# Performance work log

Hardware: AMD Instinct MI355X
Metric: run time of the kernel (lower is better)

Reference implementation:

```python
import jax, jax.numpy as jnp
import numpy as np

B, EMB, HT, WD = 32, 256, 56, 56
NH, WS, SHIFTED = 8, 4, True


def setup_inputs() -> dict:
    key = jax.random.key(0)
    ks = jax.random.split(key, 6)
    x = jax.random.normal(ks[0], (B, EMB, HT, WD), jnp.float32)
    s = 1.0 / np.sqrt(EMB)
    w1 = jax.random.uniform(ks[1], (3 * EMB, EMB), jnp.float32, -s, s)
    b1 = jax.random.uniform(ks[2], (3 * EMB,), jnp.float32, -s, s)
    w2 = jax.random.uniform(ks[3], (EMB, EMB), jnp.float32, -s, s)
    b2 = jax.random.uniform(ks[4], (EMB,), jnp.float32, -s, s)
    pos_emb = jax.random.normal(ks[5], (2 * WS - 1, 2 * WS - 1), jnp.float32)
    return {"x": x, "w1": w1, "b1": b1, "w2": w2, "b2": b2, "pos_emb": pos_emb}


def _rel_indices(ws):
    coords = np.array([[i, j] for i in range(ws) for j in range(ws)])
    rel = coords[None, :, :] - coords[:, None, :] + ws - 1  # (ws^2, ws^2, 2)
    return jnp.asarray(rel)


def _shift_masks(ws):
    m = np.zeros((ws * ws, ws * ws), np.float32)
    s = ws * (ws // 2)
    m[-s:, :-s] = -np.inf
    m[:-s, -s:] = -np.inf
    # '(r w1) (c w2) -> (w1 r) (w2 c)' with r=c=ws
    col = m.reshape(ws, ws, ws, ws).transpose(1, 0, 3, 2).reshape(ws * ws, ws * ws)
    return jnp.asarray(m), jnp.asarray(col)


def reference(x, w1, b1, w2, b2, pos_emb):
    b, c, ht, wd = x.shape
    ws, nh = WS, NH
    e = c // nh
    # b c h w -> b (h w) c, then QKV projection
    xt = x.reshape(b, c, ht * wd).transpose(0, 2, 1)
    qkv = xt @ w1.T + b1                      # (b, hw, 3c)
    # '(c k)' with c outer, k inner -> reshape (..., c, 3)
    qkv = qkv.reshape(b, ht, wd, c, 3)
    if SHIFTED:
        qkv = jnp.roll(qkv, (-ws // 2, -ws // 2), axis=(1, 2))
    Wh, Ww = ht // ws, wd // ws
    # 'b (Wh w1) (Ww w2) (e H) k -> b H Wh Ww (w1 w2) e k'  (e outer, H inner)
    qkv = qkv.reshape(b, Wh, ws, Ww, ws, e, nh, 3)
    qkv = qkv.transpose(0, 6, 1, 3, 2, 4, 5, 7).reshape(b, nh, Wh, Ww, ws * ws, e, 3)
    Q, K, V = qkv[..., 0], qkv[..., 1], qkv[..., 2]
    scale = jnp.sqrt(jnp.float32(c / nh))
    wei = jnp.einsum('bhijpe,bhijqe->bhijpq', Q, K) / scale  # (b,H,Wh,Ww,ws^2,ws^2)
    rel = _rel_indices(ws)
    wei = wei + pos_emb[rel[..., 0], rel[..., 1]]
    if SHIFTED:
        row_mask, col_mask = _shift_masks(ws)
        wei = wei.at[:, :, -1, :].add(row_mask)
        wei = wei.at[:, :, :, -1].add(col_mask)
    attn = jax.nn.softmax(wei, axis=-1)
    out = jnp.einsum('bhijpq,bhijqe->bhijpe', attn, V)
    # 'b H Wh Ww (w1 w2) e -> b (Wh w1) (Ww w2) (H e)'
    out = out.reshape(b, nh, Wh, Ww, ws, ws, e)
    out = out.transpose(0, 2, 4, 3, 5, 1, 6).reshape(b, ht, wd, nh * e)
    out = out.reshape(b, ht * wd, c)
    return out @ w2.T + b2
```

## Files before the change

### kernel.cpp

```cpp
#include <hip/hip_runtime.h>
#include <hip/hip_bf16.h>
#include <math.h>

typedef __attribute__((ext_vector_type(8))) short short8;
typedef __attribute__((ext_vector_type(4))) short short4_;
typedef __attribute__((ext_vector_type(4))) float f32x4;

#define B_    32
#define C_    256
#define HW_   3136
#define N1_   768
#define NWIN_ 14
#define M_    100352

__device__ __forceinline__ short bf16_of(float f) {
  union { __hip_bfloat16 h; short s; } u;
  u.h = __float2bfloat16(f);
  return u.s;
}

__device__ __forceinline__ void load_lds16(const void* g, void* l) {
  __builtin_amdgcn_global_load_lds(
      (const __attribute__((address_space(1))) unsigned int*)g,
      (__attribute__((address_space(3))) unsigned int*)l, 16, 0, 0);
}

__device__ __forceinline__ f32x4 mfma16x16x16bf16(short4_ a, short4_ b, f32x4 c) {
#if __has_builtin(__builtin_amdgcn_mfma_f32_16x16x16bf16_1k)
  return __builtin_amdgcn_mfma_f32_16x16x16bf16_1k(a, b, c, 0, 0, 0);
#else
  asm volatile("v_mfma_f32_16x16x16_bf16 %0, %1, %2, %0\n\ts_nop 7\n\ts_nop 7"
               : "+v"(c) : "v"(a), "v"(b));
  return c;
#endif
}

__global__ void conv_weights(const float* __restrict__ w1, const float* __restrict__ w2,
                             short* __restrict__ w1b, short* __restrict__ w2b) {
  int i = blockIdx.x * 256 + threadIdx.x;
  if (i < 196608) w1b[i] = bf16_of(w1[i]);
  if (i < 65536)  w2b[i] = bf16_of(w2[i]);
}

__global__ __launch_bounds__(256) void transpose_x(const float* __restrict__ x,
                                                   short* __restrict__ xt) {
  __shared__ short T[64 * 258];
  const int t = threadIdx.x;
  const int m0 = blockIdx.x * 64;
  const int b  = m0 / HW_;
  const int hw0 = m0 - b * HW_;

  for (int it = 0; it < 16; ++it) {
    const int c = it * 16 + (t >> 4);
    const int hw4 = (t & 15) * 4;
    float4 v = *(const float4*)(x + ((size_t)b * C_ + c) * HW_ + hw0 + hw4);
    T[(hw4 + 0) * 258 + c] = bf16_of(v.x);
    T[(hw4 + 1) * 258 + c] = bf16_of(v.y);
    T[(hw4 + 2) * 258 + c] = bf16_of(v.z);
    T[(hw4 + 3) * 258 + c] = bf16_of(v.w);
  }
  __syncthreads();
  for (int it = 0; it < 8; ++it) {
    const int idx = it * 256 + t;
    const int row = idx >> 5, ch = idx & 31;
    const short* rp = &T[row * 258 + ch * 8];
    int4 o;
    o.x = *(const int*)(rp + 0);
    o.y = *(const int*)(rp + 2);
    o.z = *(const int*)(rp + 4);
    o.w = *(const int*)(rp + 6);
    *(int4*)(xt + (size_t)(m0 + row) * C_ + ch * 8) = o;
  }
}

__global__ __launch_bounds__(256) void qkv_gemm(const short* __restrict__ xt,
    const short* __restrict__ w1b, const float* __restrict__ b1,
    short* __restrict__ qkvb) {
  __shared__ char smem[32768];
  char* As = smem;
  char* Bs = smem + 16384;
  const int t = threadIdx.x, l = t & 63, w = t >> 6;
  const int d = blockIdx.x, xcd = d & 7, i0 = d >> 3;
  const int bn = i0 % 6, bm = (i0 / 6) * 8 + xcd;
  const int m0 = bm * 128, n0 = bn * 128;
  const int lane = l & 15, kg = l >> 4;
  const int wm = w >> 1, wn = w & 1;

  f32x4 acc[4][4];
#pragma unroll
  for (int i = 0; i < 4; ++i)
#pragma unroll
    for (int j = 0; j < 4; ++j) acc[i][j] = (f32x4){0.f, 0.f, 0.f, 0.f};

  for (int ks = 0; ks < 4; ++ks) {
    const int k0 = ks * 64;
#pragma unroll
    for (int q = 0; q < 4; ++q) {
      const int row = (w * 4 + q) * 8 + (l >> 3);
      const int sc  = (l & 7) ^ (row & 7);
      load_lds16(xt  + (size_t)(m0 + row) * 256 + k0 + sc * 8, As + (w * 4 + q) * 1024);
      load_lds16(w1b + (size_t)(n0 + row) * 256 + k0 + sc * 8, Bs + (w * 4 + q) * 1024);
    }
    __syncthreads();
#pragma unroll
    for (int s = 0; s < 2; ++s) {
      short8 a[4], b[4];
#pragma unroll
      for (int i = 0; i < 4; ++i) {
        const int r = wm * 64 + i * 16 + lane;
        a[i] = *(const short8*)(As + r * 128 + ((s * 64 + kg * 16) ^ ((r & 7) << 4)));
      }
#pragma unroll
      for (int j = 0; j < 4; ++j) {
        const int r = wn * 64 + j * 16 + lane;
        b[j] = *(const short8*)(Bs + r * 128 + ((s * 64 + kg * 16) ^ ((r & 7) << 4)));
      }
#pragma unroll
      for (int i = 0; i < 4; ++i)
#pragma unroll
        for (int j = 0; j < 4; ++j)
          acc[i][j] = __builtin_amdgcn_mfma_f32_16x16x32_bf16(a[i], b[j], acc[i][j], 0, 0, 0);
    }
    __syncthreads();
  }

#pragma unroll
  for (int j = 0; j < 4; ++j) {
    const int n = n0 + wn * 64 + j * 16 + lane;
    const float bias = b1[n];
#pragma unroll
    for (int i = 0; i < 4; ++i) {
      const int mb = m0 + wm * 64 + i * 16 + kg * 4;
#pragma unroll
      for (int r = 0; r < 4; ++r)
        qkvb[(size_t)(mb + r) * N1_ + n] = bf16_of(acc[i][j][r] + bias);
    }
  }
}

__global__ __launch_bounds__(512) void win_attn(const short* __restrict__ qkvb,
    const float* __restrict__ pos, short* __restrict__ attnb) {
  __shared__ short Sq[16 * 776];
  __shared__ short Ot[16 * 272];
  __shared__ float Pe[49];

  const int t = threadIdx.x, l = t & 63, h = t >> 6;
  if (t < 49) Pe[t] = pos[t];

  const int win = blockIdx.x;
  const int wxi = win % NWIN_;
  const int wyi = (win / NWIN_) % NWIN_;
  const int b   = win / (NWIN_ * NWIN_);

#pragma unroll
  for (int rep = 0; rep < 3; ++rep) {
    const int idx = rep * 512 + t;
    const int row = idx / 96, ch = idx % 96;
    const int pr = row >> 2, pc = row & 3;
    int y  = wyi * 4 + pr + 2; if (y >= 56) y -= 56;
    int xx = wxi * 4 + pc + 2; if (xx >= 56) xx -= 56;
    const size_t m = (size_t)b * HW_ + y * 56 + xx;
    int4 v = *(const int4*)(qkvb + m * N1_ + ch * 8);
    *(int4*)(Sq + row * 776 + ch * 8) = v;
  }
  __syncthreads();

  const int lane = l & 15, kg = l >> 4;

  short8 qf, kf;
  const short* rowp = Sq + lane * 776;
#pragma unroll
  for (int j = 0; j < 8; ++j) {
    const int e = kg * 8 + j;
    const int cq = 24 * e + 3 * h;
    qf[j] = rowp[cq];
    kf[j] = rowp[cq + 1];
  }
  f32x4 z = {0.f, 0.f, 0.f, 0.f};
  f32x4 st = __builtin_amdgcn_mfma_f32_16x16x32_bf16(kf, qf, z, 0, 0, 0);

  const int pr = lane >> 2, pc = lane & 3;
  const float rscale = 0.17677669529663687f;
  float sv[4];
#pragma unroll
  for (int r = 0; r < 4; ++r) {
    const int q = kg * 4 + r, qr = q >> 2, qc = q & 3;
    float s = st[r] * rscale + Pe[(qr - pr + 3) * 7 + (qc - pc + 3)];
    if (wyi == NWIN_ - 1 && ((pr >= 2) != (qr >= 2))) s = -1e30f;
    if (wxi == NWIN_ - 1 && ((pc >= 2) != (qc >= 2))) s = -1e30f;
    sv[r] = s;
  }
  float mx = fmaxf(fmaxf(sv[0], sv[1]), fmaxf(sv[2], sv[3]));
  mx = fmaxf(mx, __shfl_xor(mx, 16));
  mx = fmaxf(mx, __shfl_xor(mx, 32));
  float ex[4], sm = 0.f;
#pragma unroll
  for (int r = 0; r < 4; ++r) { ex[r] = __expf(sv[r] - mx); sm += ex[r]; }
  sm += __shfl_xor(sm, 16);
  sm += __shfl_xor(sm, 32);
  const float inv = 1.0f / sm;
  short4_ pf;
#pragma unroll
  for (int r = 0; r < 4; ++r) pf[r] = bf16_of(ex[r] * inv);

#pragma unroll
  for (int half = 0; half < 2; ++half) {
    short4_ vf;
#pragma unroll
    for (int i = 0; i < 4; ++i) {
      const int vrow = kg * 4 + i;
      const int e = half * 16 + lane;
      vf[i] = Sq[vrow * 776 + 24 * e + 3 * h + 2];
    }
    f32x4 o = mfma16x16x16bf16(pf, vf, z);
#pragma unroll
    for (int r = 0; r < 4; ++r)
      Ot[(kg * 4 + r) * 272 + h * 32 + half * 16 + lane] = bf16_of(o[r]);
  }
  __syncthreads();

  const int row = t >> 5, ch = t & 31;
  const short* rp = &Ot[row * 272 + ch * 8];
  int4 v = *(const int4*)rp;
  const size_t mo = (size_t)b * HW_ + (wyi * 4 + (row >> 2)) * 56 + wxi * 4 + (row & 3);
  *(int4*)(attnb + mo * C_ + ch * 8) = v;
}

__global__ __launch_bounds__(256) void proj_gemm(const short* __restrict__ attnb,
    const short* __restrict__ w2b, const float* __restrict__ b2,
    float* __restrict__ out) {
  __shared__ char smem[32768];
  char* As = smem;
  char* Bs = smem + 16384;
  const int t = threadIdx.x, l = t & 63, w = t >> 6;
  const int d = blockIdx.x, xcd = d & 7, i0 = d >> 3;
  const int bn = i0 & 1, bm = (i0 >> 1) * 8 + xcd;
  const int m0 = bm * 128, n0 = bn * 128;
  const int lane = l & 15, kg = l >> 4;
  const int wm = w >> 1, wn = w & 1;

  f32x4 acc[4][4];
#pragma unroll
  for (int i = 0; i < 4; ++i)
#pragma unroll
    for (int j = 0; j < 4; ++j) acc[i][j] = (f32x4){0.f, 0.f, 0.f, 0.f};

  for (int ks = 0; ks < 4; ++ks) {
    const int k0 = ks * 64;
#pragma unroll
    for (int q = 0; q < 4; ++q) {
      const int row = (w * 4 + q) * 8 + (l >> 3);
      const int sc  = (l & 7) ^ (row & 7);
      load_lds16(attnb + (size_t)(m0 + row) * 256 + k0 + sc * 8, As + (w * 4 + q) * 1024);
      load_lds16(w2b   + (size_t)(n0 + row) * 256 + k0 + sc * 8, Bs + (w * 4 + q) * 1024);
    }
    __syncthreads();
#pragma unroll
    for (int s = 0; s < 2; ++s) {
      short8 a[4], b[4];
#pragma unroll
      for (int i = 0; i < 4; ++i) {
        const int r = wm * 64 + i * 16 + lane;
        a[i] = *(const short8*)(As + r * 128 + ((s * 64 + kg * 16) ^ ((r & 7) << 4)));
      }
#pragma unroll
      for (int j = 0; j < 4; ++j) {
        const int r = wn * 64 + j * 16 + lane;
        b[j] = *(const short8*)(Bs + r * 128 + ((s * 64 + kg * 16) ^ ((r & 7) << 4)));
      }
#pragma unroll
      for (int i = 0; i < 4; ++i)
#pragma unroll
        for (int j = 0; j < 4; ++j)
          acc[i][j] = __builtin_amdgcn_mfma_f32_16x16x32_bf16(a[i], b[j], acc[i][j], 0, 0, 0);
    }
    __syncthreads();
  }

#pragma unroll
  for (int j = 0; j < 4; ++j) {
    const int n = n0 + wn * 64 + j * 16 + lane;
    const float bias = b2[n];
#pragma unroll
    for (int i = 0; i < 4; ++i) {
      const int mb = m0 + wm * 64 + i * 16 + kg * 4;
#pragma unroll
      for (int r = 0; r < 4; ++r)
        out[(size_t)(mb + r) * C_ + n] = acc[i][j][r] + bias;
    }
  }
}

extern "C" void kernel_launch(void* const* d_in, const int* in_sizes, int n_in,
                              void* d_out, int out_size, void* d_ws, size_t ws_size,
                              hipStream_t stream) {
  const float* x   = (const float*)d_in[0];
  const float* w1  = (const float*)d_in[1];
  const float* b1  = (const float*)d_in[2];
  const float* w2  = (const float*)d_in[3];
  const float* b2  = (const float*)d_in[4];
  const float* pos = (const float*)d_in[5];
  float* out = (float*)d_out;

  char* ws = (char*)d_ws;
  short* xt    = (short*)ws;
  short* qkvb  = (short*)(ws + (size_t)52000000);
  short* attnb = (short*)(ws + (size_t)52000000 + 155000000);
  short* w1b   = (short*)(ws + (size_t)52000000 + 155000000 + 52000000);
  short* w2b   = w1b + 196608;

  conv_weights<<<768, 256, 0, stream>>>(w1, w2, w1b, w2b);
  transpose_x <<<1568, 256, 0, stream>>>(x, xt);
  qkv_gemm    <<<4704, 256, 0, stream>>>(xt, w1b, b1, qkvb);
  win_attn    <<<6272, 512, 0, stream>>>(qkvb, pos, attnb);
  proj_gemm   <<<1568, 256, 0, stream>>>(attnb, w2b, b2, out);
}
```

Baseline: 351.8 us.

## Permute QKV weight rows for contiguous Q/K/V head loads and swizzle LDS

```diff
diff --git a/kernel.cpp b/kernel.cpp
--- a/kernel.cpp
+++ b/kernel.cpp
@@ -36,45 +36,70 @@
 }
 
 __global__ void conv_weights(const float* __restrict__ w1, const float* __restrict__ w2,
-                             short* __restrict__ w1b, short* __restrict__ w2b) {
+                             const float* __restrict__ b1,
+                             short* __restrict__ w1p, short* __restrict__ w2b,
+                             float* __restrict__ b1p) {
   int i = blockIdx.x * 256 + threadIdx.x;
-  if (i < 196608) w1b[i] = bf16_of(w1[i]);
-  if (i < 65536)  w2b[i] = bf16_of(w2[i]);
+  if (i < 196608) {
+    const int r = i >> 8, c = i & 255;
+    const int k = r >> 8, rem = r & 255, h = rem >> 5, e = rem & 31;
+    const int orig = 24 * e + 3 * h + k;
+    w1p[i] = bf16_of(w1[orig * 256 + c]);
+  }
+  if (i < 65536) w2b[i] = bf16_of(w2[i]);
+  if (i < 768) {
+    const int k = i >> 8, rem = i & 255, h = rem >> 5, e = rem & 31;
+    b1p[i] = b1[24 * e + 3 * h + k];
+  }
 }
 
 __global__ __launch_bounds__(256) void transpose_x(const float* __restrict__ x,
                                                    short* __restrict__ xt) {
-  __shared__ short T[64 * 258];
+  __shared__ __align__(16) short T[64 * 256];
   const int t = threadIdx.x;
   const int m0 = blockIdx.x * 64;
   const int b  = m0 / HW_;
   const int hw0 = m0 - b * HW_;
-
-  for (int it = 0; it < 16; ++it) {
-    const int c = it * 16 + (t >> 4);
-    const int hw4 = (t & 15) * 4;
-    float4 v = *(const float4*)(x + ((size_t)b * C_ + c) * HW_ + hw0 + hw4);
-    T[(hw4 + 0) * 258 + c] = bf16_of(v.x);
-    T[(hw4 + 1) * 258 + c] = bf16_of(v.y);
-    T[(hw4 + 2) * 258 + c] = bf16_of(v.z);
-    T[(hw4 + 3) * 258 + c] = bf16_of(v.w);
+  const int tq = (t & 15) * 4;
+  const int cg = t >> 4;
+
+#pragma unroll
+  for (int p = 0; p < 4; ++p) {
+    const int cc = (p * 16 + cg) * 4;
+    const float* xp = x + ((size_t)b * C_ + cc) * HW_ + hw0 + tq;
+    float4 v0 = *(const float4*)(xp);
+    float4 v1 = *(const float4*)(xp + HW_);
+    float4 v2 = *(const float4*)(xp + 2 * HW_);
+    float4 v3 = *(const float4*)(xp + 3 * HW_);
+    const int cq = p * 16 + cg;
+#define WR_(i, e0, e1, e2, e3)                                        \
+    { const int row = tq + i;                                         \
+      short4_ wv; wv[0] = bf16_of(e0); wv[1] = bf16_of(e1);           \
+      wv[2] = bf16_of(e2); wv[3] = bf16_of(e3);                       \
+      *(short4_*)&T[row * 256 + ((cq ^ ((row >> 2) & 7)) << 2)] = wv; }
+    WR_(0, v0.x, v1.x, v2.x, v3.x)
+    WR_(1, v0.y, v1.y, v2.y, v3.y)
+    WR_(2, v0.z, v1.z, v2.z, v3.z)
+    WR_(3, v0.w, v1.w, v2.w, v3.w)
+#undef WR_
   }
   __syncthreads();
+
+#pragma unroll
   for (int it = 0; it < 8; ++it) {
     const int idx = it * 256 + t;
-    const int row = idx >> 5, ch = idx & 31;
-    const short* rp = &T[row * 258 + ch * 8];
-    int4 o;
-    o.x = *(const int*)(rp + 0);
-    o.y = *(const int*)(rp + 2);
-    o.z = *(const int*)(rp + 4);
-    o.w = *(const int*)(rp + 6);
-    *(int4*)(xt + (size_t)(m0 + row) * C_ + ch * 8) = o;
+    const int row = idx >> 5, ch16 = idx & 31;
+    const int s = (row >> 2) & 7;
+    const int cqa = (ch16 * 2) ^ s, cqb = (ch16 * 2 + 1) ^ s;
+    int2 lo = *(const int2*)&T[row * 256 + cqa * 4];
+    int2 hi = *(const int2*)&T[row * 256 + cqb * 4];
+    int4 o = make_int4(lo.x, lo.y, hi.x, hi.y);
+    *(int4*)(xt + (size_t)(m0 + row) * C_ + ch16 * 8) = o;
   }
 }
 
 __global__ __launch_bounds__(256) void qkv_gemm(const short* __restrict__ xt,
-    const short* __restrict__ w1b, const float* __restrict__ b1,
+    const short* __restrict__ w1p, const float* __restrict__ b1p,
     short* __restrict__ qkvb) {
   __shared__ char smem[32768];
   char* As = smem;
@@ -99,7 +124,7 @@
       const int row = (w * 4 + q) * 8 + (l >> 3);
       const int sc  = (l & 7) ^ (row & 7);
       load_lds16(xt  + (size_t)(m0 + row) * 256 + k0 + sc * 8, As + (w * 4 + q) * 1024);
-      load_lds16(w1b + (size_t)(n0 + row) * 256 + k0 + sc * 8, Bs + (w * 4 + q) * 1024);
+      load_lds16(w1p + (size_t)(n0 + row) * 256 + k0 + sc * 8, Bs + (w * 4 + q) * 1024);
     }
     __syncthreads();
 #pragma unroll
@@ -127,7 +152,7 @@
 #pragma unroll
   for (int j = 0; j < 4; ++j) {
     const int n = n0 + wn * 64 + j * 16 + lane;
-    const float bias = b1[n];
+    const float bias = b1p[n];
 #pragma unroll
     for (int i = 0; i < 4; ++i) {
       const int mb = m0 + wm * 64 + i * 16 + kg * 4;
@@ -140,8 +165,8 @@
 
 __global__ __launch_bounds__(512) void win_attn(const short* __restrict__ qkvb,
     const float* __restrict__ pos, short* __restrict__ attnb) {
-  __shared__ short Sq[16 * 776];
-  __shared__ short Ot[16 * 272];
+  __shared__ __align__(16) short Sq[16 * 768];
+  __shared__ __align__(16) short Ot[16 * 272];
   __shared__ float Pe[49];
 
   const int t = threadIdx.x, l = t & 63, h = t >> 6;
@@ -161,21 +186,16 @@
     int xx = wxi * 4 + pc + 2; if (xx >= 56) xx -= 56;
     const size_t m = (size_t)b * HW_ + y * 56 + xx;
     int4 v = *(const int4*)(qkvb + m * N1_ + ch * 8);
-    *(int4*)(Sq + row * 776 + ch * 8) = v;
+    *(int4*)(Sq + row * 768 + (ch ^ (row & 7)) * 8) = v;
   }
   __syncthreads();
 
   const int lane = l & 15, kg = l >> 4;
 
-  short8 qf, kf;
-  const short* rowp = Sq + lane * 776;
-#pragma unroll
-  for (int j = 0; j < 8; ++j) {
-    const int e = kg * 8 + j;
-    const int cq = 24 * e + 3 * h;
-    qf[j] = rowp[cq];
-    kf[j] = rowp[cq + 1];
-  }
+  const int cQ = h * 4 + kg;
+  short8 qf = *(const short8*)(Sq + lane * 768 + ((cQ)      ^ (lane & 7)) * 8);
+  short8 kf = *(const short8*)(Sq + lane * 768 + ((32 + cQ) ^ (lane & 7)) * 8);
+
   f32x4 z = {0.f, 0.f, 0.f, 0.f};
   f32x4 st = __builtin_amdgcn_mfma_f32_16x16x32_bf16(kf, qf, z, 0, 0, 0);
 
@@ -206,11 +226,12 @@
 #pragma unroll
   for (int half = 0; half < 2; ++half) {
     short4_ vf;
+    const int cV = 64 + h * 4 + half * 2 + (lane >> 3);
+    const int el = lane & 7;
 #pragma unroll
     for (int i = 0; i < 4; ++i) {
       const int vrow = kg * 4 + i;
-      const int e = half * 16 + lane;
-      vf[i] = Sq[vrow * 776 + 24 * e + 3 * h + 2];
+      vf[i] = Sq[vrow * 768 + (cV ^ (vrow & 7)) * 8 + el];
     }
     f32x4 o = mfma16x16x16bf16(pf, vf, z);
 #pragma unroll
@@ -306,12 +327,13 @@
   short* xt    = (short*)ws;
   short* qkvb  = (short*)(ws + (size_t)52000000);
   short* attnb = (short*)(ws + (size_t)52000000 + 155000000);
-  short* w1b   = (short*)(ws + (size_t)52000000 + 155000000 + 52000000);
-  short* w2b   = w1b + 196608;
-
-  conv_weights<<<768, 256, 0, stream>>>(w1, w2, w1b, w2b);
+  short* w1p   = (short*)(ws + (size_t)52000000 + 155000000 + 52000000);
+  short* w2b   = w1p + 196608;
+  float* b1p   = (float*)(w2b + 65536);
+
+  conv_weights<<<768, 256, 0, stream>>>(w1, w2, b1, w1p, w2b, b1p);
   transpose_x <<<1568, 256, 0, stream>>>(x, xt);
-  qkv_gemm    <<<4704, 256, 0, stream>>>(xt, w1b, b1, qkvb);
+  qkv_gemm    <<<4704, 256, 0, stream>>>(xt, w1p, b1p, qkvb);
   win_attn    <<<6272, 512, 0, stream>>>(qkvb, pos, attnb);
   proj_gemm   <<<1568, 256, 0, stream>>>(attnb, w2b, b2, out);
 }
```

After: 349.8 us. Within noise of the previous version (-0.5%).
